# Kernel tuning notes

Hardware: AMD Instinct MI355X
Metric: run time of the kernel (lower is better)

The kernel has to match this reference:

```python
import jax, jax.numpy as jnp
import numpy as np

D_MODEL = 1024
N_HEADS = 16
HEAD_DIM = D_MODEL // N_HEADS


def setup_inputs() -> dict:
    key = jax.random.key(0)
    ks = jax.random.split(key, 9)
    s = 1.0 / np.sqrt(D_MODEL)
    mk = lambda k: jax.random.uniform(k, (D_MODEL, D_MODEL), jnp.float32, -s, s)
    mb = lambda k: jax.random.uniform(k, (D_MODEL,), jnp.float32, -s, s)
    return {
        "x": jax.random.normal(ks[0], (2, 2048, D_MODEL), jnp.float32),
        "Wq": mk(ks[1]), "bq": mb(ks[2]),
        "Wk": mk(ks[3]), "bk": mb(ks[4]),
        "Wv": mk(ks[5]), "bv": mb(ks[6]),
        "Wo": mk(ks[7]), "bo": mb(ks[8]),
    }


def _split_heads(t, B, S):
    # [B,S,D] -> [B,H,S,hd]
    return t.reshape(B, S, N_HEADS, HEAD_DIM).transpose(0, 2, 1, 3)


def reference(x, Wq, bq, Wk, bk, Wv, bv, Wo, bo):
    B, S, _ = x.shape
    # torch Linear: y = x @ W.T + b  (W stored [out, in])
    Q = _split_heads(x @ Wq.T + bq, B, S)
    K = _split_heads(x @ Wk.T + bk, B, S)
    V = _split_heads(x @ Wv.T + bv, B, S)
    scores = jnp.einsum("bhsd,bhtd->bhst", Q, K) / np.sqrt(HEAD_DIM).astype(np.float32)
    attn = jax.nn.softmax(scores, axis=-1)
    out = jnp.einsum("bhst,bhtd->bhsd", attn, V)
    out = out.transpose(0, 2, 1, 3).reshape(B, S, D_MODEL)
    return out @ Wo.T + bo
```

## Files before the change

### kernel.cpp

```cpp
#include <hip/hip_runtime.h>
#include <math.h>

#define D_MODEL 1024
#define NH 16
#define HD 64
#define SEQ 2048
#define NB 2
#define BSROWS (NB * SEQ)
#define NT (SEQ / 64)

typedef __attribute__((ext_vector_type(8)))  short short8;
typedef __attribute__((ext_vector_type(4)))  float f32x4;
typedef __attribute__((ext_vector_type(16))) float f32x16;

__device__ __forceinline__ ushort bf16rne(float f) {
    union { float f; uint32_t u; } v; v.f = f;
    return (ushort)((v.u + 0x7FFFu + ((v.u >> 16) & 1u)) >> 16);
}

__device__ __forceinline__ void gl_lds16(const void* g, void* l) {
    __builtin_amdgcn_global_load_lds(
        reinterpret_cast<const uint32_t __attribute__((address_space(1)))*>(
            reinterpret_cast<uintptr_t>(g)),
        reinterpret_cast<uint32_t __attribute__((address_space(3)))*>(
            reinterpret_cast<uintptr_t>(l)),
        16, 0, 0);
}

__global__ __launch_bounds__(256) void convert_x(const float* __restrict__ in,
                                                 ushort* __restrict__ out) {
    const int i = blockIdx.x * 256 + threadIdx.x;
    const float4 a = ((const float4*)in)[2 * i];
    const float4 b = ((const float4*)in)[2 * i + 1];
    union { ushort u[8]; uint4 v; } r;
    r.u[0] = bf16rne(a.x); r.u[1] = bf16rne(a.y); r.u[2] = bf16rne(a.z); r.u[3] = bf16rne(a.w);
    r.u[4] = bf16rne(b.x); r.u[5] = bf16rne(b.y); r.u[6] = bf16rne(b.z); r.u[7] = bf16rne(b.w);
    ((uint4*)out)[i] = r.v;
}

__global__ __launch_bounds__(256) void convert_w(const float* __restrict__ w0,
                                                 const float* __restrict__ w1,
                                                 const float* __restrict__ w2,
                                                 const float* __restrict__ w3,
                                                 ushort* __restrict__ qkv,
                                                 ushort* __restrict__ wo) {
    const int which = blockIdx.y;
    const float* src = (which == 0) ? w0 : (which == 1) ? w1 : (which == 2) ? w2 : w3;
    ushort* dst = (which < 3) ? (qkv + (size_t)which * D_MODEL * D_MODEL) : wo;
    const int i = blockIdx.x * 256 + threadIdx.x;
    const float4 a = ((const float4*)src)[2 * i];
    const float4 b = ((const float4*)src)[2 * i + 1];
    union { ushort u[8]; uint4 v; } r;
    r.u[0] = bf16rne(a.x); r.u[1] = bf16rne(a.y); r.u[2] = bf16rne(a.z); r.u[3] = bf16rne(a.w);
    r.u[4] = bf16rne(b.x); r.u[5] = bf16rne(b.y); r.u[6] = bf16rne(b.z); r.u[7] = bf16rne(b.w);
    ((uint4*)dst)[i] = r.v;
}

template <int BN, int MODE>
__global__ __launch_bounds__(256) void gemm_mfma(const ushort* __restrict__ A,
                                                 const ushort* __restrict__ B,
                                                 const float* __restrict__ b0,
                                                 const float* __restrict__ b1,
                                                 const float* __restrict__ b2,
                                                 void* __restrict__ o0v,
                                                 void* __restrict__ o1v,
                                                 void* __restrict__ o2v) {
    constexpr int BM = 128, BK = 32;
    constexpr int WN = (BN == 128) ? 64 : 32;
    constexpr int NM = 4;
    constexpr int NN = WN / 16;

    __shared__ ushort As[BM * BK];
    __shared__ ushort Bs[BN * BK];

    const int tid = threadIdx.x;
    const int w   = tid >> 6;
    const int l   = tid & 63;
    const int i0  = blockIdx.x * BM;
    const int n0  = blockIdx.y * BN;

    const int wr = (w >> 1) * 64;
    const int wc = (w & 1) * WN;

    const int srow = l >> 2;
    const int scol = (l & 3) * 8;
    const ushort* ga = A + (size_t)(i0 + w * 32 + srow) * D_MODEL + scol;
    const ushort* gb = B + (size_t)(n0 + w * (BN / 4) + srow) * D_MODEL + scol;
    ushort* lA = &As[(w * 32) * BK];
    ushort* lB = &Bs[(w * (BN / 4)) * BK];

    f32x4 acc[NM][NN];
#pragma unroll
    for (int m = 0; m < NM; ++m)
#pragma unroll
        for (int n = 0; n < NN; ++n) acc[m][n] = (f32x4){0.f, 0.f, 0.f, 0.f};

    const int fr = l & 15;
    const int kc = (l >> 4) * 8;

    for (int k0 = 0; k0 < D_MODEL; k0 += BK) {
        __syncthreads();
        gl_lds16(ga, lA);
        gl_lds16(ga + 16 * D_MODEL, lA + 16 * BK);
        gl_lds16(gb, lB);
        if (BN == 128) gl_lds16(gb + 16 * D_MODEL, lB + 16 * BK);
        ga += BK; gb += BK;
        __syncthreads();

        short8 af[NM], bfr[NN];
#pragma unroll
        for (int m = 0; m < NM; ++m)
            af[m] = *(const short8*)&As[(wr + m * 16 + fr) * BK + kc];
#pragma unroll
        for (int n = 0; n < NN; ++n)
            bfr[n] = *(const short8*)&Bs[(wc + n * 16 + fr) * BK + kc];
#pragma unroll
        for (int m = 0; m < NM; ++m)
#pragma unroll
            for (int n = 0; n < NN; ++n)
                acc[m][n] = __builtin_amdgcn_mfma_f32_16x16x32_bf16(af[m], bfr[n], acc[m][n], 0, 0, 0);
    }

    const int rr = (l >> 4) * 4;

    if (MODE == 1) {
        float* out = (float*)o0v;
#pragma unroll
        for (int n = 0; n < NN; ++n) {
            const int j = n0 + wc + n * 16 + fr;
            const float bj = b0[j];
#pragma unroll
            for (int m = 0; m < NM; ++m) {
                const int row = i0 + wr + m * 16 + rr;
#pragma unroll
                for (int r = 0; r < 4; ++r)
                    out[(size_t)(row + r) * D_MODEL + j] = acc[m][n][r] + bj;
            }
        }
    } else {
        const int p = n0 >> 10;
        const float* bias = (p == 0) ? b0 : (p == 1) ? b1 : b2;
        const float scl = (p == 0) ? 0.125f : 1.0f;
#pragma unroll
        for (int n = 0; n < NN; ++n) {
            const int j = n0 + wc + n * 16 + fr;
            const int f = j & 1023;
            const float bj = bias[f];
            const int h = f >> 6, d = f & 63;
#pragma unroll
            for (int m = 0; m < NM; ++m) {
                const int row = i0 + wr + m * 16 + rr;
                const int bb = row >> 11;
                const int s0 = row & (SEQ - 1);
                if (p < 2) {
                    ushort* dst = (ushort*)(p == 0 ? o0v : o1v);
#pragma unroll
                    for (int r = 0; r < 4; ++r)
                        dst[(((size_t)bb * NH + h) * SEQ + (s0 + r)) * HD + d] =
                            bf16rne((acc[m][n][r] + bj) * scl);
                } else {
                    ushort4 pk;
                    pk.x = bf16rne(acc[m][n][0] + bj);
                    pk.y = bf16rne(acc[m][n][1] + bj);
                    pk.z = bf16rne(acc[m][n][2] + bj);
                    pk.w = bf16rne(acc[m][n][3] + bj);
                    *(ushort4*)&((ushort*)o2v)[(((size_t)bb * NH + h) * HD + d) * SEQ + s0] = pk;
                }
            }
        }
    }
}

__global__ __launch_bounds__(256) void attn_mfma3(const ushort* __restrict__ Q,
                                                  const ushort* __restrict__ K,
                                                  const ushort* __restrict__ Vt,
                                                  ushort* __restrict__ Aout) {
    __shared__ ushort KsB[2 * 4096];
    __shared__ ushort VtsB[2 * 4096];

    const int tid = threadIdx.x;
    const int w   = tid >> 6;
    const int l   = tid & 63;
    const int lq  = l & 31;
    const int hi  = l >> 5;
    const int qt  = blockIdx.x;
    const int h   = blockIdx.y;
    const int b   = blockIdx.z;
    const size_t bh = (size_t)b * NH + h;

    const ushort* Qg = Q  + (bh * SEQ + (size_t)qt * 128 + w * 32 + lq) * HD;
    const ushort* Kg = K  + bh * SEQ * HD;
    const ushort* Vg = Vt + bh * HD * SEQ;

    short8 qf[4];
#pragma unroll
    for (int dk = 0; dk < 4; ++dk)
        qf[dk] = *(const short8*)&Qg[dk * 16 + hi * 8];

    int srow[2], scol[2], ssw[2];
#pragma unroll
    for (int j = 0; j < 2; ++j) {
        const int idx = tid + j * 256;
        srow[j] = idx >> 3;
        scol[j] = (idx & 7) * 8;
        ssw[j]  = scol[j] ^ ((srow[j] & 7) << 3);
    }

    uint4 kreg[2], vreg[2];
#pragma unroll
    for (int j = 0; j < 2; ++j) {
        kreg[j] = *(const uint4*)&Kg[(size_t)srow[j] * HD + scol[j]];
        vreg[j] = *(const uint4*)&Vg[(size_t)srow[j] * SEQ + scol[j]];
    }
#pragma unroll
    for (int j = 0; j < 2; ++j) {
        *(uint4*)&KsB [srow[j] * 64 + ssw[j]] = kreg[j];
        *(uint4*)&VtsB[srow[j] * 64 + ssw[j]] = vreg[j];
    }
    __syncthreads();

    f32x16 oa0, oa1;
#pragma unroll
    for (int r = 0; r < 16; ++r) { oa0[r] = 0.f; oa1[r] = 0.f; }
    float m = -3.0e38f, lsum = 0.f;

    for (int kt = 0; kt < NT; ++kt) {
        const ushort* Ks  = &KsB [(kt & 1) * 4096];
        const ushort* Vts = &VtsB[(kt & 1) * 4096];
        ushort* Ksn  = &KsB [((kt + 1) & 1) * 4096];
        ushort* Vtsn = &VtsB[((kt + 1) & 1) * 4096];

        if (kt + 1 < NT) {
#pragma unroll
            for (int j = 0; j < 2; ++j) {
                kreg[j] = *(const uint4*)&Kg[((size_t)(kt + 1) * 64 + srow[j]) * HD + scol[j]];
                vreg[j] = *(const uint4*)&Vg[(size_t)srow[j] * SEQ + (kt + 1) * 64 + scol[j]];
            }
        }

        f32x16 sc0, sc1;
#pragma unroll
        for (int r = 0; r < 16; ++r) { sc0[r] = 0.f; sc1[r] = 0.f; }
        const int ksw0 = (lq & 7) << 3;
        __builtin_amdgcn_s_setprio(1);
#pragma unroll
        for (int dk = 0; dk < 4; ++dk) {
            const int col = (dk * 16 + hi * 8) ^ ksw0;
            const short8 kf0 = *(const short8*)&Ks[lq * 64 + col];
            const short8 kf1 = *(const short8*)&Ks[(32 + lq) * 64 + col];
            sc0 = __builtin_amdgcn_mfma_f32_32x32x16_bf16(kf0, qf[dk], sc0, 0, 0, 0);
            sc1 = __builtin_amdgcn_mfma_f32_32x32x16_bf16(kf1, qf[dk], sc1, 0, 0, 0);
        }
        __builtin_amdgcn_s_setprio(0);

        float t0 = fmaxf(fmaxf(sc0[0], sc0[1]), fmaxf(sc0[2], sc0[3]));
        float t1 = fmaxf(fmaxf(sc0[4], sc0[5]), fmaxf(sc0[6], sc0[7]));
        float t2 = fmaxf(fmaxf(sc0[8], sc0[9]), fmaxf(sc0[10], sc0[11]));
        float t3 = fmaxf(fmaxf(sc0[12], sc0[13]), fmaxf(sc0[14], sc0[15]));
        float u0 = fmaxf(fmaxf(sc1[0], sc1[1]), fmaxf(sc1[2], sc1[3]));
        float u1 = fmaxf(fmaxf(sc1[4], sc1[5]), fmaxf(sc1[6], sc1[7]));
        float u2 = fmaxf(fmaxf(sc1[8], sc1[9]), fmaxf(sc1[10], sc1[11]));
        float u3 = fmaxf(fmaxf(sc1[12], sc1[13]), fmaxf(sc1[14], sc1[15]));
        float pm = fmaxf(fmaxf(fmaxf(t0, t1), fmaxf(t2, t3)),
                         fmaxf(fmaxf(u0, u1), fmaxf(u2, u3)));
        pm = fmaxf(pm, __shfl_xor(pm, 32));

        if (!__all(pm - m <= 8.0f)) {
            const float mn = fmaxf(m, pm);
            const float corr = __expf(m - mn);
            m = mn; lsum *= corr;
#pragma unroll
            for (int r = 0; r < 16; ++r) { oa0[r] *= corr; oa1[r] *= corr; }
        }

        float p0[16], p1[16];
#pragma unroll
        for (int r = 0; r < 16; ++r) { p0[r] = __expf(sc0[r] - m); p1[r] = __expf(sc1[r] - m); }
        lsum += (((p0[0] + p0[1]) + (p0[2] + p0[3])) + ((p0[4] + p0[5]) + (p0[6] + p0[7])))
              + (((p0[8] + p0[9]) + (p0[10] + p0[11])) + ((p0[12] + p0[13]) + (p0[14] + p0[15])))
              + (((p1[0] + p1[1]) + (p1[2] + p1[3])) + ((p1[4] + p1[5]) + (p1[6] + p1[7])))
              + (((p1[8] + p1[9]) + (p1[10] + p1[11])) + ((p1[12] + p1[13]) + (p1[14] + p1[15])));

        uint32_t pk0[8], pk1[8], x0[8], x1[8];
#pragma unroll
        for (int i = 0; i < 8; ++i) {
            asm("v_cvt_pk_bf16_f32 %0, %1, %2" : "=v"(pk0[i]) : "v"(p0[2 * i]), "v"(p0[2 * i + 1]));
            asm("v_cvt_pk_bf16_f32 %0, %1, %2" : "=v"(pk1[i]) : "v"(p1[2 * i]), "v"(p1[2 * i + 1]));
        }
#pragma unroll
        for (int i = 0; i < 8; ++i) { x0[i] = __shfl_xor(pk0[i], 32); x1[i] = __shfl_xor(pk1[i], 32); }

        union U8 { uint32_t u[4]; short8 s; };
        U8 a0, a1, b0, b1;
        a0.u[0] = hi ? x0[2]  : pk0[0];  a0.u[1] = hi ? x0[3]  : pk0[1];
        a0.u[2] = hi ? pk0[2] : x0[0];   a0.u[3] = hi ? pk0[3] : x0[1];
        a1.u[0] = hi ? x0[6]  : pk0[4];  a1.u[1] = hi ? x0[7]  : pk0[5];
        a1.u[2] = hi ? pk0[6] : x0[4];   a1.u[3] = hi ? pk0[7] : x0[5];
        b0.u[0] = hi ? x1[2]  : pk1[0];  b0.u[1] = hi ? x1[3]  : pk1[1];
        b0.u[2] = hi ? pk1[2] : x1[0];   b0.u[3] = hi ? pk1[3] : x1[1];
        b1.u[0] = hi ? x1[6]  : pk1[4];  b1.u[1] = hi ? x1[7]  : pk1[5];
        b1.u[2] = hi ? pk1[6] : x1[4];   b1.u[3] = hi ? pk1[7] : x1[5];
        const short8 pf00 = a0.s, pf01 = a1.s, pf10 = b0.s, pf11 = b1.s;

        const int d0 = lq, d1 = 32 + lq;
        const int vsw0 = (d0 & 7) << 3;
        const int tA = hi * 8;
        const short8 vA0 = *(const short8*)&Vts[d0 * 64 + ((tA)      ^ vsw0)];
        const short8 vA1 = *(const short8*)&Vts[d1 * 64 + ((tA)      ^ vsw0)];
        const short8 vB0 = *(const short8*)&Vts[d0 * 64 + ((tA + 16) ^ vsw0)];
        const short8 vB1 = *(const short8*)&Vts[d1 * 64 + ((tA + 16) ^ vsw0)];
        const short8 wA0 = *(const short8*)&Vts[d0 * 64 + ((tA + 32) ^ vsw0)];
        const short8 wA1 = *(const short8*)&Vts[d1 * 64 + ((tA + 32) ^ vsw0)];
        const short8 wB0 = *(const short8*)&Vts[d0 * 64 + ((tA + 48) ^ vsw0)];
        const short8 wB1 = *(const short8*)&Vts[d1 * 64 + ((tA + 48) ^ vsw0)];
        __builtin_amdgcn_s_setprio(1);
        oa0 = __builtin_amdgcn_mfma_f32_32x32x16_bf16(vA0, pf00, oa0, 0, 0, 0);
        oa1 = __builtin_amdgcn_mfma_f32_32x32x16_bf16(vA1, pf00, oa1, 0, 0, 0);
        oa0 = __builtin_amdgcn_mfma_f32_32x32x16_bf16(vB0, pf01, oa0, 0, 0, 0);
        oa1 = __builtin_amdgcn_mfma_f32_32x32x16_bf16(vB1, pf01, oa1, 0, 0, 0);
        oa0 = __builtin_amdgcn_mfma_f32_32x32x16_bf16(wA0, pf10, oa0, 0, 0, 0);
        oa1 = __builtin_amdgcn_mfma_f32_32x32x16_bf16(wA1, pf10, oa1, 0, 0, 0);
        oa0 = __builtin_amdgcn_mfma_f32_32x32x16_bf16(wB0, pf11, oa0, 0, 0, 0);
        oa1 = __builtin_amdgcn_mfma_f32_32x32x16_bf16(wB1, pf11, oa1, 0, 0, 0);
        __builtin_amdgcn_s_setprio(0);

        if (kt + 1 < NT) {
#pragma unroll
            for (int j = 0; j < 2; ++j) {
                *(uint4*)&Ksn [srow[j] * 64 + ssw[j]] = kreg[j];
                *(uint4*)&Vtsn[srow[j] * 64 + ssw[j]] = vreg[j];
            }
        }
        __syncthreads();
    }

    lsum += __shfl_xor(lsum, 32);
    const float inv = 1.f / lsum;

    ushort* Ow = KsB + w * 2048;
#pragma unroll
    for (int r = 0; r < 16; ++r) {
        const int dd = (r & 3) + 8 * (r >> 2) + 4 * hi;
        const int swq = (lq & 7) << 3;
        Ow[lq * 64 + ((dd)      ^ swq)] = bf16rne(oa0[r] * inv);
        Ow[lq * 64 + ((dd + 32) ^ swq)] = bf16rne(oa1[r] * inv);
    }
    const size_t orow0 = (size_t)b * SEQ + (size_t)qt * 128 + w * 32;
#pragma unroll
    for (int i = 0; i < 4; ++i) {
        const int row = (l >> 3) + 8 * i;
        const int d0 = (l & 7) * 8;
        const uint4 v = *(const uint4*)&Ow[row * 64 + (d0 ^ ((row & 7) << 3))];
        *(uint4*)&Aout[(orow0 + row) * D_MODEL + h * HD + d0] = v;
    }
}

extern "C" void kernel_launch(void* const* d_in, const int* in_sizes, int n_in,
                              void* d_out, int out_size, void* d_ws, size_t ws_size,
                              hipStream_t stream) {
    const float* x  = (const float*)d_in[0];
    const float* Wq = (const float*)d_in[1];
    const float* bq = (const float*)d_in[2];
    const float* Wk = (const float*)d_in[3];
    const float* bk = (const float*)d_in[4];
    const float* Wv = (const float*)d_in[5];
    const float* bv = (const float*)d_in[6];
    const float* Wo = (const float*)d_in[7];
    const float* bo = (const float*)d_in[8];
    float* out = (float*)d_out;

    ushort* xb   = (ushort*)d_ws;
    ushort* Wqkv = xb   + (size_t)BSROWS * D_MODEL;
    ushort* Wob  = Wqkv + (size_t)3 * D_MODEL * D_MODEL;
    ushort* Qw   = Wob  + (size_t)D_MODEL * D_MODEL;
    ushort* Kw   = Qw   + (size_t)BSROWS * D_MODEL;
    ushort* Vw   = Kw   + (size_t)BSROWS * D_MODEL;
    ushort* Ab   = Vw   + (size_t)BSROWS * D_MODEL;

    convert_w<<<dim3(512, 4), 256, 0, stream>>>(Wq, Wk, Wv, Wo, Wqkv, Wob);
    convert_x<<<dim3(2048), 256, 0, stream>>>(x, xb);

    gemm_mfma<128, 0><<<dim3(32, 24), 256, 0, stream>>>(
        xb, Wqkv, bq, bk, bv, Qw, Kw, Vw);

    attn_mfma3<<<dim3(SEQ / 128, NH, NB), 256, 0, stream>>>(Qw, Kw, Vw, Ab);

    gemm_mfma<64, 1><<<dim3(32, 16), 256, 0, stream>>>(
        Ab, Wob, bo, nullptr, nullptr, out, nullptr, nullptr);
}
```

Baseline: 144.3 us.

## Split attention KV range across two wave groups and merge partial softmax states

The attention kernel now launches 512 threads per block. Two groups of four waves each process half of the key/value tiles for the same 128 query rows, then merge their partial outputs, running maxima and sums through shared memory with a rescaled combine. This doubles the waves available per query tile, which increases latency hiding and occupancy for a grid of only 512 blocks. The cost is a shared-memory reduction, extra syncs, and doubled LDS use per block (64KB), which may limit how many blocks fit per CU.

```diff
diff --git a/kernel.cpp b/kernel.cpp
--- a/kernel.cpp
+++ b/kernel.cpp
@@ -171,15 +171,18 @@
     }
 }
 
-__global__ __launch_bounds__(256) void attn_mfma3(const ushort* __restrict__ Q,
-                                                  const ushort* __restrict__ K,
-                                                  const ushort* __restrict__ Vt,
-                                                  ushort* __restrict__ Aout) {
-    __shared__ ushort KsB[2 * 4096];
-    __shared__ ushort VtsB[2 * 4096];
+__global__ __launch_bounds__(512, 4) void attn_mfma4(const ushort* __restrict__ Q,
+                                                     const ushort* __restrict__ K,
+                                                     const ushort* __restrict__ Vt,
+                                                     ushort* __restrict__ Aout) {
+    __shared__ ushort smem[32768];
+    ushort* KsB  = smem;
+    ushort* VtsB = smem + 16384;
 
     const int tid = threadIdx.x;
     const int w   = tid >> 6;
+    const int grp = w >> 2;
+    const int wq  = w & 3;
     const int l   = tid & 63;
     const int lq  = l & 31;
     const int hi  = l >> 5;
@@ -188,7 +191,7 @@
     const int b   = blockIdx.z;
     const size_t bh = (size_t)b * NH + h;
 
-    const ushort* Qg = Q  + (bh * SEQ + (size_t)qt * 128 + w * 32 + lq) * HD;
+    const ushort* Qg = Q  + (bh * SEQ + (size_t)qt * 128 + wq * 32 + lq) * HD;
     const ushort* Kg = K  + bh * SEQ * HD;
     const ushort* Vg = Vt + bh * HD * SEQ;
 
@@ -197,25 +200,30 @@
     for (int dk = 0; dk < 4; ++dk)
         qf[dk] = *(const short8*)&Qg[dk * 16 + hi * 8];
 
+    const int gtid = tid & 255;
     int srow[2], scol[2], ssw[2];
 #pragma unroll
     for (int j = 0; j < 2; ++j) {
-        const int idx = tid + j * 256;
+        const int idx = gtid + j * 256;
         srow[j] = idx >> 3;
         scol[j] = (idx & 7) * 8;
         ssw[j]  = scol[j] ^ ((srow[j] & 7) << 3);
     }
+    ushort* KsG  = KsB  + grp * 8192;
+    ushort* VtsG = VtsB + grp * 8192;
+
+    const int kt0 = grp * 16, kt1 = kt0 + 16;
 
     uint4 kreg[2], vreg[2];
 #pragma unroll
     for (int j = 0; j < 2; ++j) {
-        kreg[j] = *(const uint4*)&Kg[(size_t)srow[j] * HD + scol[j]];
-        vreg[j] = *(const uint4*)&Vg[(size_t)srow[j] * SEQ + scol[j]];
+        kreg[j] = *(const uint4*)&Kg[((size_t)kt0 * 64 + srow[j]) * HD + scol[j]];
+        vreg[j] = *(const uint4*)&Vg[(size_t)srow[j] * SEQ + kt0 * 64 + scol[j]];
     }
 #pragma unroll
     for (int j = 0; j < 2; ++j) {
-        *(uint4*)&KsB [srow[j] * 64 + ssw[j]] = kreg[j];
-        *(uint4*)&VtsB[srow[j] * 64 + ssw[j]] = vreg[j];
+        *(uint4*)&KsG [srow[j] * 64 + ssw[j]] = kreg[j];
+        *(uint4*)&VtsG[srow[j] * 64 + ssw[j]] = vreg[j];
     }
     __syncthreads();
 
@@ -224,13 +232,14 @@
     for (int r = 0; r < 16; ++r) { oa0[r] = 0.f; oa1[r] = 0.f; }
     float m = -3.0e38f, lsum = 0.f;
 
-    for (int kt = 0; kt < NT; ++kt) {
-        const ushort* Ks  = &KsB [(kt & 1) * 4096];
-        const ushort* Vts = &VtsB[(kt & 1) * 4096];
-        ushort* Ksn  = &KsB [((kt + 1) & 1) * 4096];
-        ushort* Vtsn = &VtsB[((kt + 1) & 1) * 4096];
-
-        if (kt + 1 < NT) {
+    for (int kt = kt0; kt < kt1; ++kt) {
+        const int buf = (kt - kt0) & 1;
+        const ushort* Ks  = KsG  + buf * 4096;
+        const ushort* Vts = VtsG + buf * 4096;
+        ushort* Ksn  = KsG  + (buf ^ 1) * 4096;
+        ushort* Vtsn = VtsG + (buf ^ 1) * 4096;
+
+        if (kt + 1 < kt1) {
 #pragma unroll
             for (int j = 0; j < 2; ++j) {
                 kreg[j] = *(const uint4*)&Kg[((size_t)(kt + 1) * 64 + srow[j]) * HD + scol[j]];
@@ -324,7 +333,7 @@
         oa1 = __builtin_amdgcn_mfma_f32_32x32x16_bf16(wB1, pf11, oa1, 0, 0, 0);
         __builtin_amdgcn_s_setprio(0);
 
-        if (kt + 1 < NT) {
+        if (kt + 1 < kt1) {
 #pragma unroll
             for (int j = 0; j < 2; ++j) {
                 *(uint4*)&Ksn [srow[j] * 64 + ssw[j]] = kreg[j];
@@ -335,23 +344,47 @@
     }
 
     lsum += __shfl_xor(lsum, 32);
-    const float inv = 1.f / lsum;
-
-    ushort* Ow = KsB + w * 2048;
+
+    __syncthreads();
+    float* mb = (float*)(smem + 8192);
+    float* myexp = mb + ((size_t)w * 64 + l) * 19;
+    {
+        const f32x16& ex = (grp == 0) ? oa1 : oa0;
+#pragma unroll
+        for (int r = 0; r < 16; ++r) myexp[r] = ex[r];
+        myexp[16] = m; myexp[17] = lsum;
+    }
+    __syncthreads();
+    const float* pexp = mb + ((size_t)(w ^ 4) * 64 + l) * 19;
+    const float pmv = pexp[16], plv = pexp[17];
+    const float M   = fmaxf(m, pmv);
+    const float cs  = __expf(m - M);
+    const float cp  = __expf(pmv - M);
+    const float inv = 1.f / (lsum * cs + plv * cp);
+
+    f32x16 om;
+    {
+        const f32x16& keep = (grp == 0) ? oa0 : oa1;
+#pragma unroll
+        for (int r = 0; r < 16; ++r) om[r] = (keep[r] * cs + pexp[r] * cp) * inv;
+    }
+
+    ushort* Ow = smem + wq * 2048;
+    const int dbase = grp * 32;
+    const int swq = (lq & 7) << 3;
 #pragma unroll
     for (int r = 0; r < 16; ++r) {
-        const int dd = (r & 3) + 8 * (r >> 2) + 4 * hi;
-        const int swq = (lq & 7) << 3;
-        Ow[lq * 64 + ((dd)      ^ swq)] = bf16rne(oa0[r] * inv);
-        Ow[lq * 64 + ((dd + 32) ^ swq)] = bf16rne(oa1[r] * inv);
-    }
-    const size_t orow0 = (size_t)b * SEQ + (size_t)qt * 128 + w * 32;
-#pragma unroll
-    for (int i = 0; i < 4; ++i) {
-        const int row = (l >> 3) + 8 * i;
-        const int d0 = (l & 7) * 8;
-        const uint4 v = *(const uint4*)&Ow[row * 64 + (d0 ^ ((row & 7) << 3))];
-        *(uint4*)&Aout[(orow0 + row) * D_MODEL + h * HD + d0] = v;
+        const int dd = (r & 3) + 8 * (r >> 2) + 4 * hi + dbase;
+        Ow[lq * 64 + (dd ^ swq)] = bf16rne(om[r]);
+    }
+    __syncthreads();
+    const size_t orow0 = (size_t)b * SEQ + (size_t)qt * 128 + wq * 32;
+#pragma unroll
+    for (int i = 0; i < 2; ++i) {
+        const int rowl = grp * 16 + (l >> 3) + 8 * i;
+        const int dc = (l & 7) * 8;
+        const uint4 v = *(const uint4*)&Ow[rowl * 64 + (dc ^ ((rowl & 7) << 3))];
+        *(uint4*)&Aout[(orow0 + rowl) * D_MODEL + h * HD + dc] = v;
     }
 }
 
@@ -383,7 +416,7 @@
     gemm_mfma<128, 0><<<dim3(32, 24), 256, 0, stream>>>(
         xb, Wqkv, bq, bk, bv, Qw, Kw, Vw);
 
-    attn_mfma3<<<dim3(SEQ / 128, NH, NB), 256, 0, stream>>>(Qw, Kw, Vw, Ab);
+    attn_mfma4<<<dim3(SEQ / 128, NH, NB), 512, 0, stream>>>(Qw, Kw, Vw, Ab);
 
     gemm_mfma<64, 1><<<dim3(32, 16), 256, 0, stream>>>(
         Ab, Wob, bo, nullptr, nullptr, out, nullptr, nullptr);
```

Measured after the change: 286.9 us. 1.99x slower.

## Split attention over two KV halves and merge partials with log-sum-exp

Applied to the files above, without the earlier changes.

The attention kernel is split along the key dimension into two halves, which doubles the grid from 512 to 1024 blocks so more CUs stay busy. Each half writes fp16 normalized partial outputs plus per-row (max, sum) stats. A new merge kernel combines the two halves with softmax rescaling and writes the bf16 output for the projection GEMM. This costs an extra launch and extra global traffic for the partials, and the stats buffer reuses the x workspace, which is no longer needed at that point.

```diff
diff --git a/kernel.cpp b/kernel.cpp
--- a/kernel.cpp
+++ b/kernel.cpp
@@ -1,4 +1,5 @@
 #include <hip/hip_runtime.h>
+#include <hip/hip_fp16.h>
 #include <math.h>
 
 #define D_MODEL 1024
@@ -171,21 +172,23 @@
     }
 }
 
-__global__ __launch_bounds__(256) void attn_mfma3(const ushort* __restrict__ Q,
+__global__ __launch_bounds__(256) void attn_mfma5(const ushort* __restrict__ Q,
                                                   const ushort* __restrict__ K,
                                                   const ushort* __restrict__ Vt,
-                                                  ushort* __restrict__ Aout) {
+                                                  ushort* __restrict__ Opart,
+                                                  float2* __restrict__ stats) {
     __shared__ ushort KsB[2 * 4096];
     __shared__ ushort VtsB[2 * 4096];
 
-    const int tid = threadIdx.x;
-    const int w   = tid >> 6;
-    const int l   = tid & 63;
-    const int lq  = l & 31;
-    const int hi  = l >> 5;
-    const int qt  = blockIdx.x;
-    const int h   = blockIdx.y;
-    const int b   = blockIdx.z;
+    const int tid  = threadIdx.x;
+    const int w    = tid >> 6;
+    const int l    = tid & 63;
+    const int lq   = l & 31;
+    const int hi   = l >> 5;
+    const int qt   = blockIdx.x;
+    const int h    = blockIdx.y;
+    const int b    = blockIdx.z & 1;
+    const int half = blockIdx.z >> 1;
     const size_t bh = (size_t)b * NH + h;
 
     const ushort* Qg = Q  + (bh * SEQ + (size_t)qt * 128 + w * 32 + lq) * HD;
@@ -206,11 +209,13 @@
         ssw[j]  = scol[j] ^ ((srow[j] & 7) << 3);
     }
 
+    const int kt0 = half * 16, kt1 = kt0 + 16;
+
     uint4 kreg[2], vreg[2];
 #pragma unroll
     for (int j = 0; j < 2; ++j) {
-        kreg[j] = *(const uint4*)&Kg[(size_t)srow[j] * HD + scol[j]];
-        vreg[j] = *(const uint4*)&Vg[(size_t)srow[j] * SEQ + scol[j]];
+        kreg[j] = *(const uint4*)&Kg[((size_t)kt0 * 64 + srow[j]) * HD + scol[j]];
+        vreg[j] = *(const uint4*)&Vg[(size_t)srow[j] * SEQ + kt0 * 64 + scol[j]];
     }
 #pragma unroll
     for (int j = 0; j < 2; ++j) {
@@ -224,13 +229,14 @@
     for (int r = 0; r < 16; ++r) { oa0[r] = 0.f; oa1[r] = 0.f; }
     float m = -3.0e38f, lsum = 0.f;
 
-    for (int kt = 0; kt < NT; ++kt) {
-        const ushort* Ks  = &KsB [(kt & 1) * 4096];
-        const ushort* Vts = &VtsB[(kt & 1) * 4096];
-        ushort* Ksn  = &KsB [((kt + 1) & 1) * 4096];
-        ushort* Vtsn = &VtsB[((kt + 1) & 1) * 4096];
-
-        if (kt + 1 < NT) {
+    for (int kt = kt0; kt < kt1; ++kt) {
+        const int buf = (kt - kt0) & 1;
+        const ushort* Ks  = &KsB [buf * 4096];
+        const ushort* Vts = &VtsB[buf * 4096];
+        ushort* Ksn  = &KsB [(buf ^ 1) * 4096];
+        ushort* Vtsn = &VtsB[(buf ^ 1) * 4096];
+
+        if (kt + 1 < kt1) {
 #pragma unroll
             for (int j = 0; j < 2; ++j) {
                 kreg[j] = *(const uint4*)&Kg[((size_t)(kt + 1) * 64 + srow[j]) * HD + scol[j]];
@@ -324,7 +330,7 @@
         oa1 = __builtin_amdgcn_mfma_f32_32x32x16_bf16(wB1, pf11, oa1, 0, 0, 0);
         __builtin_amdgcn_s_setprio(0);
 
-        if (kt + 1 < NT) {
+        if (kt + 1 < kt1) {
 #pragma unroll
             for (int j = 0; j < 2; ++j) {
                 *(uint4*)&Ksn [srow[j] * 64 + ssw[j]] = kreg[j];
@@ -337,22 +343,58 @@
     lsum += __shfl_xor(lsum, 32);
     const float inv = 1.f / lsum;
 
+    const size_t srow0 = (((size_t)half * NB + b) * NH + h) * SEQ + (size_t)qt * 128 + w * 32;
+    if (l < 32) stats[srow0 + lq] = make_float2(m, lsum);
+
     ushort* Ow = KsB + w * 2048;
+    const int swq = (lq & 7) << 3;
 #pragma unroll
     for (int r = 0; r < 16; ++r) {
         const int dd = (r & 3) + 8 * (r >> 2) + 4 * hi;
-        const int swq = (lq & 7) << 3;
-        Ow[lq * 64 + ((dd)      ^ swq)] = bf16rne(oa0[r] * inv);
-        Ow[lq * 64 + ((dd + 32) ^ swq)] = bf16rne(oa1[r] * inv);
-    }
-    const size_t orow0 = (size_t)b * SEQ + (size_t)qt * 128 + w * 32;
+        Ow[lq * 64 + ((dd)      ^ swq)] = __half_as_ushort(__float2half_rn(oa0[r] * inv));
+        Ow[lq * 64 + ((dd + 32) ^ swq)] = __half_as_ushort(__float2half_rn(oa1[r] * inv));
+    }
+    __syncthreads();
 #pragma unroll
     for (int i = 0; i < 4; ++i) {
         const int row = (l >> 3) + 8 * i;
-        const int d0 = (l & 7) * 8;
-        const uint4 v = *(const uint4*)&Ow[row * 64 + (d0 ^ ((row & 7) << 3))];
-        *(uint4*)&Aout[(orow0 + row) * D_MODEL + h * HD + d0] = v;
-    }
+        const int dc = (l & 7) * 8;
+        const uint4 v = *(const uint4*)&Ow[row * 64 + (dc ^ ((row & 7) << 3))];
+        *(uint4*)&Opart[(srow0 + row) * HD + dc] = v;
+    }
+}
+
+__global__ __launch_bounds__(256) void attn_merge(const ushort* __restrict__ Opart,
+                                                  const float2* __restrict__ stats,
+                                                  ushort* __restrict__ Ab) {
+    const int g   = blockIdx.x * 256 + threadIdx.x;
+    const int d8  = (g & 7) * 8;
+    const int h   = (g >> 3) & 15;
+    const int row = g >> 7;
+    const int b   = row >> 11;
+    const int s   = row & (SEQ - 1);
+
+    const size_t sbase = ((size_t)b * NH + h) * SEQ + s;
+    const size_t sstr  = (size_t)NB * NH * SEQ;
+    const float2 s0 = stats[sbase];
+    const float2 s1 = stats[sbase + sstr];
+    const float M  = fmaxf(s0.x, s1.x);
+    const float w0 = s0.y * __expf(s0.x - M);
+    const float w1 = s1.y * __expf(s1.x - M);
+    const float inv = 1.f / (w0 + w1);
+    const float a0 = w0 * inv, a1 = w1 * inv;
+
+    const size_t pbase = sbase * HD + d8;
+    const uint4 u0 = *(const uint4*)&Opart[pbase];
+    const uint4 u1 = *(const uint4*)&Opart[pbase + sstr * HD];
+    const ushort* h0 = (const ushort*)&u0;
+    const ushort* h1 = (const ushort*)&u1;
+    union { ushort u[8]; uint4 v; } o;
+#pragma unroll
+    for (int i = 0; i < 8; ++i)
+        o.u[i] = bf16rne(a0 * __half2float(__ushort_as_half(h0[i])) +
+                         a1 * __half2float(__ushort_as_half(h1[i])));
+    *(uint4*)&Ab[(size_t)row * D_MODEL + h * HD + d8] = o.v;
 }
 
 extern "C" void kernel_launch(void* const* d_in, const int* in_sizes, int n_in,
@@ -369,13 +411,16 @@
     const float* bo = (const float*)d_in[8];
     float* out = (float*)d_out;
 
-    ushort* xb   = (ushort*)d_ws;
-    ushort* Wqkv = xb   + (size_t)BSROWS * D_MODEL;
-    ushort* Wob  = Wqkv + (size_t)3 * D_MODEL * D_MODEL;
-    ushort* Qw   = Wob  + (size_t)D_MODEL * D_MODEL;
-    ushort* Kw   = Qw   + (size_t)BSROWS * D_MODEL;
-    ushort* Vw   = Kw   + (size_t)BSROWS * D_MODEL;
-    ushort* Ab   = Vw   + (size_t)BSROWS * D_MODEL;
+    ushort* ws16 = (ushort*)d_ws;
+    ushort* xb    = ws16;
+    float2* stats = (float2*)d_ws;
+    ushort* Wqkv  = ws16 + (size_t)BSROWS * D_MODEL;
+    ushort* Wob   = Wqkv + (size_t)3 * D_MODEL * D_MODEL;
+    ushort* Qw    = Wob  + (size_t)D_MODEL * D_MODEL;
+    ushort* Kw    = Qw   + (size_t)BSROWS * D_MODEL;
+    ushort* Vw    = Kw   + (size_t)BSROWS * D_MODEL;
+    ushort* Ab    = Vw   + (size_t)BSROWS * D_MODEL;
+    ushort* Opart = Ab   + (size_t)BSROWS * D_MODEL;
 
     convert_w<<<dim3(512, 4), 256, 0, stream>>>(Wq, Wk, Wv, Wo, Wqkv, Wob);
     convert_x<<<dim3(2048), 256, 0, stream>>>(x, xb);
@@ -383,7 +428,9 @@
     gemm_mfma<128, 0><<<dim3(32, 24), 256, 0, stream>>>(
         xb, Wqkv, bq, bk, bv, Qw, Kw, Vw);
 
-    attn_mfma3<<<dim3(SEQ / 128, NH, NB), 256, 0, stream>>>(Qw, Kw, Vw, Ab);
+    attn_mfma5<<<dim3(SEQ / 128, NH, NB * 2), 256, 0, stream>>>(
+        Qw, Kw, Vw, Opart, stats);
+    attn_merge<<<dim3(2048), 256, 0, stream>>>(Opart, stats, Ab);
 
     gemm_mfma<64, 1><<<dim3(32, 16), 256, 0, stream>>>(
         Ab, Wob, bo, nullptr, nullptr, out, nullptr, nullptr);
```

Result: slower. 176.3 us (+22.2%).
